# Performance work log

Hardware: AMD Instinct MI355X
Metric: run time of the kernel (lower is better)

## Reference

```python
import jax, jax.numpy as jnp
import numpy as np

N = 20000        # nodes
E = 160000       # directed edges (before self loops)
NODE_DIM = 1287
HEADS = 4
C1, C2, C3 = 128, 256, 128
ACT_SLOPE = 0.15   # module's LeakyReLU between layers
GAT_SLOPE = 0.2    # PyG GATConv default negative_slope


def _gat_layer(x, src, dst, W, att_src, att_dst, bias, heads, out_dim, concat):
    # x: [N, in] ; W: [in, heads*out] ; att_*: [heads, out] ; bias: [heads*out] or [out]
    h = (x @ W).reshape(N, heads, out_dim)                      # [N, H, C]
    a_s = jnp.einsum('nhc,hc->nh', h, att_src)                  # [N, H]
    a_d = jnp.einsum('nhc,hc->nh', h, att_dst)                  # [N, H]
    e = jax.nn.leaky_relu(a_s[src] + a_d[dst], GAT_SLOPE)       # [Etot, H]
    # segment softmax over incoming edges of each dst node (self loops => no empty segments)
    m = jax.ops.segment_max(e, dst, num_segments=N)             # [N, H]
    w = jnp.exp(e - m[dst])
    den = jax.ops.segment_sum(w, dst, num_segments=N)           # [N, H]
    alpha = w / den[dst]                                        # [Etot, H]
    msg = h[src] * alpha[:, :, None]                            # [Etot, H, C]
    out = jax.ops.segment_sum(msg, dst, num_segments=N)         # [N, H, C]
    out = out.reshape(N, heads * out_dim) if concat else out.mean(axis=1)
    return out + bias


def setup_inputs() -> dict:
    key = jax.random.key(0)
    ks = jax.random.split(key, 22)
    s = 0.05
    x = jax.random.normal(ks[0], (N, NODE_DIM), jnp.float32)
    edge_index = jax.random.randint(ks[1], (2, E), 0, N, dtype=jnp.int64)
    inp = {
        'x': x, 'edge_index': edge_index,
        'W1': jax.random.normal(ks[2], (NODE_DIM, HEADS * C1), jnp.float32) * s,
        'as1': jax.random.normal(ks[3], (HEADS, C1), jnp.float32) * s,
        'ad1': jax.random.normal(ks[4], (HEADS, C1), jnp.float32) * s,
        'b1': jnp.zeros((HEADS * C1,), jnp.float32),
        'W2': jax.random.normal(ks[5], (HEADS * C1, HEADS * C2), jnp.float32) * s,
        'as2': jax.random.normal(ks[6], (HEADS, C2), jnp.float32) * s,
        'ad2': jax.random.normal(ks[7], (HEADS, C2), jnp.float32) * s,
        'b2': jnp.zeros((HEADS * C2,), jnp.float32),
        # conv3: 1024 -> 128, 1 head, no concat
        'W3': jax.random.normal(ks[8], (HEADS * C2, C3), jnp.float32) * s,
        'as3': jax.random.normal(ks[9], (1, C3), jnp.float32) * s,
        'ad3': jax.random.normal(ks[10], (1, C3), jnp.float32) * s,
        'b3': jnp.zeros((C3,), jnp.float32),
        # pre_fc: 128 -> 16
        'pw': jax.random.normal(ks[11], (C3, 16), jnp.float32) * s,
        'pb': jnp.zeros((16,), jnp.float32),
        # fc fallback: Linear(16,32) -> LeakyReLU(0.15) -> Linear(32,2)
        'f1w': jax.random.normal(ks[12], (16, 32), jnp.float32) * s,
        'f1b': jnp.zeros((32,), jnp.float32),
        'f2w': jax.random.normal(ks[13], (32, 2), jnp.float32) * s,
        'f2b': jnp.zeros((2,), jnp.float32),
    }
    return inp


def reference(x, edge_index, W1, as1, ad1, b1, W2, as2, ad2, b2,
              W3, as3, ad3, b3, pw, pb, f1w, f1b, f2w, f2b):
    loop = jnp.arange(N, dtype=edge_index.dtype)
    src = jnp.concatenate([edge_index[0], loop])   # PyG add_self_loops=True
    dst = jnp.concatenate([edge_index[1], loop])
    h = _gat_layer(x, src, dst, W1, as1, ad1, b1, HEADS, C1, True)
    h = jax.nn.leaky_relu(h, ACT_SLOPE)            # dropout = identity (eval)
    h = _gat_layer(h, src, dst, W2, as2, ad2, b2, HEADS, C2, True)
    h = jax.nn.leaky_relu(h, ACT_SLOPE)
    h = _gat_layer(h, src, dst, W3, as3, ad3, b3, 1, C3, False)
    h = jax.nn.leaky_relu(h, ACT_SLOPE)
    h = h @ pw + pb                                 # pre_fc (128 -> 16)
    h = jax.nn.leaky_relu(h @ f1w + f1b, ACT_SLOPE)
    return h @ f2w + f2b                            # [N, 2] logits
```

## Files before the change

### kernel.cpp

```cpp
#include <hip/hip_runtime.h>
#include <hip/hip_bf16.h>
#include <cstdint>
#include <cstddef>

#define LRELU(x, s) ((x) > 0.f ? (x) : (s) * (x))

typedef __attribute__((ext_vector_type(8))) short bf16x8;
typedef __attribute__((ext_vector_type(4))) float f32x4;

__device__ __forceinline__ float bflo(uint v) { return __uint_as_float(v << 16); }
__device__ __forceinline__ float bfhi(uint v) { return __uint_as_float(v & 0xffff0000u); }
__device__ __forceinline__ ushort f2bf(float f) {
  const uint u = __float_as_uint(f);
  return (ushort)((u + 0x7fffu + ((u >> 16) & 1u)) >> 16);
}

__global__ void cast_pad_rows(const float* __restrict__ in, ushort* __restrict__ out,
                              int rows, int K, int Kp) {
  const int P4 = Kp >> 2;
  const long long idx = (long long)blockIdx.x * blockDim.x + threadIdx.x;
  if (idx >= (long long)rows * P4) return;
  const int r = (int)(idx / P4);
  const int c = ((int)(idx - (long long)r * P4)) << 2;
  const float* p = in + (size_t)r * K + c;
  float v0 = 0.f, v1 = 0.f, v2 = 0.f, v3 = 0.f;
  if (c + 3 < K) { v0 = p[0]; v1 = p[1]; v2 = p[2]; v3 = p[3]; }
  else {
    if (c + 0 < K) v0 = p[0];
    if (c + 1 < K) v1 = p[1];
    if (c + 2 < K) v2 = p[2];
    if (c + 3 < K) v3 = p[3];
  }
  uint2 o;
  o.x = (uint)f2bf(v0) | ((uint)f2bf(v1) << 16);
  o.y = (uint)f2bf(v2) | ((uint)f2bf(v3) << 16);
  *(uint2*)(out + (size_t)r * Kp + c) = o;
}

__global__ void cast_W_T(const float* __restrict__ W, ushort* __restrict__ Wt,
                         int K, int Nn, int Kp) {
  __shared__ float tile[32][33];
  const int kt = blockIdx.x * 32;
  const int nt = blockIdx.y * 32;
  const int tx = threadIdx.x;
  const int ty = threadIdx.y;
  for (int r = ty; r < 32; r += 8) {
    const int k = kt + r, nn = nt + tx;
    tile[r][tx] = (k < K && nn < Nn) ? W[(size_t)k * Nn + nn] : 0.f;
  }
  __syncthreads();
  for (int r = ty; r < 32; r += 8) {
    const int nn = nt + r, k = kt + tx;
    if (nn < Nn && k < Kp) Wt[(size_t)nn * Kp + k] = f2bf(tile[tx][r]);
  }
}

__global__ __launch_bounds__(256) void gemm_bf16(
    const ushort* __restrict__ A, const ushort* __restrict__ Bt, ushort* __restrict__ C,
    int M, int N, int Kp) {
  constexpr int LDA = 40;
  __shared__ ushort sA[128 * LDA];
  __shared__ ushort sB[128 * LDA];
  const int tid = threadIdx.x;
  const int wave = tid >> 6;
  const int lane = tid & 63;
  const int tilesN = N >> 7;
  const int bx = blockIdx.x % tilesN;
  const int by = blockIdx.x / tilesN;
  const int srow = tid >> 2;
  const int sseg = (tid & 3) * 8;
  const int wrow = (wave >> 1) * 64;
  const int wcol = (wave & 1) * 64;
  const int quad = lane >> 4;
  const int ml = lane & 15;

  const int rA1 = min(by * 128 + srow, M - 1);
  const int rA2 = min(by * 128 + srow + 64, M - 1);
  const int cB1 = bx * 128 + srow;
  const size_t offA1 = (size_t)rA1 * Kp + sseg;
  const size_t offA2 = (size_t)rA2 * Kp + sseg;
  const size_t offB1 = (size_t)cB1 * Kp + sseg;
  const size_t offB2 = (size_t)(cB1 + 64) * Kp + sseg;

  f32x4 acc[4][4];
#pragma unroll
  for (int mi = 0; mi < 4; mi++)
#pragma unroll
    for (int ni = 0; ni < 4; ni++)
#pragma unroll
      for (int e = 0; e < 4; e++) acc[mi][ni][e] = 0.f;

  for (int k0 = 0; k0 < Kp; k0 += 32) {
    const uint4 a1 = *(const uint4*)(A + offA1 + k0);
    const uint4 a2 = *(const uint4*)(A + offA2 + k0);
    const uint4 b1 = *(const uint4*)(Bt + offB1 + k0);
    const uint4 b2 = *(const uint4*)(Bt + offB2 + k0);
    __syncthreads();
    *(uint4*)&sA[srow * LDA + sseg] = a1;
    *(uint4*)&sA[(srow + 64) * LDA + sseg] = a2;
    *(uint4*)&sB[srow * LDA + sseg] = b1;
    *(uint4*)&sB[(srow + 64) * LDA + sseg] = b2;
    __syncthreads();
    bf16x8 af[4], bfr[4];
#pragma unroll
    for (int mi = 0; mi < 4; mi++)
      af[mi] = *(const bf16x8*)&sA[(wrow + mi * 16 + ml) * LDA + quad * 8];
#pragma unroll
    for (int ni = 0; ni < 4; ni++)
      bfr[ni] = *(const bf16x8*)&sB[(wcol + ni * 16 + ml) * LDA + quad * 8];
#pragma unroll
    for (int mi = 0; mi < 4; mi++)
#pragma unroll
      for (int ni = 0; ni < 4; ni++)
        acc[mi][ni] = __builtin_amdgcn_mfma_f32_16x16x32_bf16(af[mi], bfr[ni], acc[mi][ni], 0, 0, 0);
  }

#pragma unroll
  for (int mi = 0; mi < 4; mi++) {
#pragma unroll
    for (int r = 0; r < 4; r++) {
      const int row = by * 128 + wrow + mi * 16 + quad * 4 + r;
      if (row < M) {
#pragma unroll
        for (int ni = 0; ni < 4; ni++) {
          const int col = bx * 128 + wcol + ni * 16 + ml;
          C[(size_t)row * N + col] = f2bf(acc[mi][ni][r]);
        }
      }
    }
  }
}

__global__ void count_deg(const int* __restrict__ dst, int E, int* __restrict__ deg) {
  const int t = blockIdx.x * blockDim.x + threadIdx.x;
  if (t < E) atomicAdd(&deg[dst[t]], 1);
}

__global__ __launch_bounds__(1024) void scan_kernel(const int* __restrict__ deg,
                                                    int* __restrict__ rowptr,
                                                    int* __restrict__ cursor, int n) {
  __shared__ int swsum[16];
  __shared__ int carry_s;
  const int t = threadIdx.x;
  const int wv = t >> 6, lane = t & 63;
  if (t == 0) carry_s = 0;
  __syncthreads();
  for (int base = 0; base < n; base += 1024) {
    const int i = base + t;
    const int v = (i < n) ? (deg[i] + 1) : 0;
    int sc = v;
#pragma unroll
    for (int off = 1; off < 64; off <<= 1) {
      const int u = __shfl_up(sc, off);
      if (lane >= off) sc += u;
    }
    if (lane == 63) swsum[wv] = sc;
    __syncthreads();
    if (t < 16) {
      int x = swsum[t];
#pragma unroll
      for (int off = 1; off < 16; off <<= 1) {
        const int u = __shfl_up(x, off);
        if (t >= off) x += u;
      }
      swsum[t] = x;
    }
    __syncthreads();
    const int incl = sc + (wv == 0 ? 0 : swsum[wv - 1]) + carry_s;
    if (i < n) { rowptr[i + 1] = incl; cursor[i] = incl - v; }
    if (base == 0 && t == 0) rowptr[0] = 0;
    __syncthreads();
    if (t == 0) carry_s += swsum[15];
    __syncthreads();
  }
}

__global__ void scatter_edges(const int* __restrict__ esrc, const int* __restrict__ edst,
                              int E, int Etot, int* __restrict__ cursor,
                              int* __restrict__ csr_src) {
  const int t = blockIdx.x * blockDim.x + threadIdx.x;
  if (t >= Etot) return;
  int s, d;
  if (t < E) { s = esrc[t]; d = edst[t]; } else { s = t - E; d = s; }
  const int pos = atomicAdd(&cursor[d], 1);
  csr_src[pos] = s;
}

template <int H, int C>
__global__ void att_dots_b(const ushort* __restrict__ hb, const float* __restrict__ att_s,
                           const float* __restrict__ att_d, float* __restrict__ a_s,
                           float* __restrict__ a_d, int NH) {
  const int w = blockIdx.x * (blockDim.x >> 6) + (threadIdx.x >> 6);
  const int lane = threadIdx.x & 63;
  if (w >= NH) return;
  const int n = w / H;
  const int h = w - n * H;
  const uint* hp = (const uint*)(hb + (size_t)n * (H * C) + h * C);
  const float2* asp = (const float2*)(att_s + h * C);
  const float2* adp = (const float2*)(att_d + h * C);
  float ss = 0.f, sd = 0.f;
#pragma unroll
  for (int p = lane; p < C / 2; p += 64) {
    const uint v = hp[p];
    const float x0 = bflo(v), x1 = bfhi(v);
    const float2 a = asp[p], b = adp[p];
    ss += x0 * a.x + x1 * a.y;
    sd += x0 * b.x + x1 * b.y;
  }
  for (int off = 32; off > 0; off >>= 1) {
    ss += __shfl_down(ss, off);
    sd += __shfl_down(sd, off);
  }
  if (lane == 0) { a_s[w] = ss; a_d[w] = sd; }
}

template <int H, int C, int TPB, int PPT>
__global__ __launch_bounds__(TPB) void gat_aggregate_b(
    const ushort* __restrict__ hb, const int* __restrict__ rowptr,
    const int* __restrict__ csr_src, const float* __restrict__ a_s,
    const float* __restrict__ a_d, const float* __restrict__ bias,
    ushort* __restrict__ outb, float act_slope) {
  constexpr int HC = H * C;
  constexpr int CH = C / 2;
  constexpr int TILE = 32;
  const int n = blockIdx.x;
  const int tid = threadIdx.x;
  __shared__ int ssrc[TILE];
  __shared__ float sw[TILE * H];
  __shared__ float sden[H];
  if (tid < H) sden[tid] = 0.f;
  float ad_n[H];
#pragma unroll
  for (int h = 0; h < H; h++) ad_n[h] = a_d[n * H + h];
  const int start = rowptr[n], end = rowptr[n + 1];
  float2 acc[PPT];
#pragma unroll
  for (int q = 0; q < PPT; q++) acc[q] = make_float2(0.f, 0.f);

  for (int base = start; base < end; base += TILE) {
    const int cnt = min(TILE, end - base);
    __syncthreads();
    if (tid < cnt) {
      const int s = csr_src[base + tid];
      ssrc[tid] = s;
      float asv[H];
      if constexpr (H == 4) {
        const float4 t4 = *(const float4*)(a_s + s * 4);
        asv[0] = t4.x; asv[1] = t4.y; asv[2] = t4.z; asv[3] = t4.w;
      } else {
#pragma unroll
        for (int h = 0; h < H; h++) asv[h] = a_s[s * H + h];
      }
#pragma unroll
      for (int h = 0; h < H; h++) {
        float lg = asv[h] + ad_n[h];
        lg = LRELU(lg, 0.2f);
        const float w = __expf(lg);
        sw[tid * H + h] = w;
        atomicAdd(&sden[h], w);
      }
    }
    __syncthreads();
    for (int j = 0; j < cnt; j++) {
      const uint* hp = (const uint*)(hb + (size_t)ssrc[j] * HC);
      const float* swj = &sw[j * H];
#pragma unroll
      for (int q = 0; q < PPT; q++) {
        const int p = tid + q * TPB;
        const float w = swj[p / CH];
        const uint v = hp[p];
        acc[q].x += w * bflo(v);
        acc[q].y += w * bfhi(v);
      }
    }
  }
  __syncthreads();
  if (tid < H) sden[tid] = 1.f / sden[tid];
  __syncthreads();
#pragma unroll
  for (int q = 0; q < PPT; q++) {
    const int p = tid + q * TPB;
    const float iv = sden[p / CH];
    const float2 b2 = *(const float2*)(bias + 2 * p);
    const float v0 = LRELU(acc[q].x * iv + b2.x, act_slope);
    const float v1 = LRELU(acc[q].y * iv + b2.y, act_slope);
    ((uint*)outb)[(size_t)n * (HC / 2) + p] = (uint)f2bf(v0) | ((uint)f2bf(v1) << 16);
  }
}

__global__ __launch_bounds__(64) void gat_agg3_mlp(
    const ushort* __restrict__ hb, const int* __restrict__ rowptr,
    const int* __restrict__ csr_src, const float* __restrict__ a_s,
    const float* __restrict__ a_d, const float* __restrict__ b3,
    const float* __restrict__ pw, const float* __restrict__ pb,
    const float* __restrict__ f1w, const float* __restrict__ f1b,
    const float* __restrict__ f2w, const float* __restrict__ f2b,
    float* __restrict__ out) {
  constexpr int TILE = 32;
  const int n = blockIdx.x;
  const int tid = threadIdx.x;
  __shared__ int ssrc[TILE];
  __shared__ float sw[TILE];
  __shared__ float sden1;
  __shared__ float sx[128];
  __shared__ float s1[16];
  __shared__ float s2[32];
  if (tid == 0) sden1 = 0.f;
  const float ad_n = a_d[n];
  const int start = rowptr[n], end = rowptr[n + 1];
  float2 acc = make_float2(0.f, 0.f);
  for (int base = start; base < end; base += TILE) {
    const int cnt = min(TILE, end - base);
    __syncthreads();
    if (tid < cnt) {
      const int s = csr_src[base + tid];
      ssrc[tid] = s;
      float lg = a_s[s] + ad_n;
      lg = LRELU(lg, 0.2f);
      const float w = __expf(lg);
      sw[tid] = w;
      atomicAdd(&sden1, w);
    }
    __syncthreads();
    for (int j = 0; j < cnt; j++) {
      const uint v = ((const uint*)(hb + (size_t)ssrc[j] * 128))[tid];
      const float w = sw[j];
      acc.x += w * bflo(v);
      acc.y += w * bfhi(v);
    }
  }
  __syncthreads();
  const float iv = 1.f / sden1;
  sx[2 * tid]     = LRELU(acc.x * iv + b3[2 * tid], 0.15f);
  sx[2 * tid + 1] = LRELU(acc.y * iv + b3[2 * tid + 1], 0.15f);
  __syncthreads();
  if (tid < 16) {
    float a = pb[tid];
    for (int c = 0; c < 128; c++) a += sx[c] * pw[c * 16 + tid];
    s1[tid] = a;
  }
  __syncthreads();
  if (tid < 32) {
    float a = f1b[tid];
    for (int c = 0; c < 16; c++) a += s1[c] * f1w[c * 32 + tid];
    s2[tid] = LRELU(a, 0.15f);
  }
  __syncthreads();
  if (tid < 2) {
    float a = f2b[tid];
    for (int c = 0; c < 32; c++) a += s2[c] * f2w[c * 2 + tid];
    out[(size_t)n * 2 + tid] = a;
  }
}

extern "C" void kernel_launch(void* const* d_in, const int* in_sizes, int n_in,
                              void* d_out, int out_size, void* d_ws, size_t ws_size,
                              hipStream_t stream) {
  const float* x   = (const float*)d_in[0];
  const int* ei    = (const int*)d_in[1];
  const float* W1  = (const float*)d_in[2];
  const float* as1 = (const float*)d_in[3];
  const float* ad1 = (const float*)d_in[4];
  const float* b1  = (const float*)d_in[5];
  const float* W2  = (const float*)d_in[6];
  const float* as2 = (const float*)d_in[7];
  const float* ad2 = (const float*)d_in[8];
  const float* b2  = (const float*)d_in[9];
  const float* W3  = (const float*)d_in[10];
  const float* as3 = (const float*)d_in[11];
  const float* ad3 = (const float*)d_in[12];
  const float* b3  = (const float*)d_in[13];
  const float* pw  = (const float*)d_in[14];
  const float* pb  = (const float*)d_in[15];
  const float* f1w = (const float*)d_in[16];
  const float* f1b = (const float*)d_in[17];
  const float* f2w = (const float*)d_in[18];
  const float* f2b = (const float*)d_in[19];
  float* out = (float*)d_out;

  const int N = in_sizes[0] / 1287;
  const int E = in_sizes[1] / 2;
  const int Etot = E + N;
  const int* esrc = ei;
  const int* edst = ei + E;
  const int K1 = 1287, K1p = 1312;

  char* ws = (char*)d_ws;
  size_t off = 0;
  auto alloc = [&](size_t bytes) -> void* {
    void* p = ws + off;
    off = (off + bytes + 255) & ~(size_t)255;
    return p;
  };
  ushort* hb  = (ushort*)alloc((size_t)N * 1024 * 2);
  ushort* ob  = (ushort*)alloc((size_t)N * 1024 * 2);
  ushort* xb  = (ushort*)alloc((size_t)N * K1p * 2);
  ushort* W1t = (ushort*)alloc((size_t)512 * K1p * 2);
  ushort* W2t = (ushort*)alloc((size_t)1024 * 512 * 2);
  ushort* W3t = (ushort*)alloc((size_t)128 * 1024 * 2);
  float* as_buf = (float*)alloc((size_t)N * 4 * sizeof(float));
  float* ad_buf = (float*)alloc((size_t)N * 4 * sizeof(float));
  int* deg    = (int*)alloc((size_t)N * sizeof(int));
  int* rowptr = (int*)alloc((size_t)(N + 1) * sizeof(int));
  int* cursor = (int*)alloc((size_t)N * sizeof(int));
  int* csr    = (int*)alloc((size_t)Etot * sizeof(int));

  hipMemsetAsync(deg, 0, (size_t)N * sizeof(int), stream);
  count_deg<<<(E + 255) / 256, 256, 0, stream>>>(edst, E, deg);
  scan_kernel<<<1, 1024, 0, stream>>>(deg, rowptr, cursor, N);
  scatter_edges<<<(Etot + 255) / 256, 256, 0, stream>>>(esrc, edst, E, Etot, cursor, csr);

  {
    const long long nx = (long long)N * (K1p / 4);
    cast_pad_rows<<<(int)((nx + 255) / 256), 256, 0, stream>>>(x, xb, N, K1, K1p);
    cast_W_T<<<dim3(K1p / 32, (512 + 31) / 32), dim3(32, 8), 0, stream>>>(W1, W1t, K1, 512, K1p);
    cast_W_T<<<dim3(512 / 32, 1024 / 32), dim3(32, 8), 0, stream>>>(W2, W2t, 512, 1024, 512);
    cast_W_T<<<dim3(1024 / 32, 128 / 32), dim3(32, 8), 0, stream>>>(W3, W3t, 1024, 128, 1024);
  }

  const int tilesM = (N + 127) / 128;

  {
    const int H = 4, C = 128, HC = 512;
    gemm_bf16<<<tilesM * (HC / 128), 256, 0, stream>>>(xb, W1t, hb, N, HC, K1p);
    const int NH = N * H;
    att_dots_b<4, 128><<<(NH + 3) / 4, 256, 0, stream>>>(hb, as1, ad1, as_buf, ad_buf, NH);
    gat_aggregate_b<4, 128, 256, 1><<<N, 256, 0, stream>>>(hb, rowptr, csr, as_buf, ad_buf,
                                                           b1, ob, 0.15f);
  }
  {
    const int H = 4, C = 256, HC = 1024;
    gemm_bf16<<<tilesM * (HC / 128), 256, 0, stream>>>(ob, W2t, hb, N, HC, 512);
    const int NH = N * H;
    att_dots_b<4, 256><<<(NH + 3) / 4, 256, 0, stream>>>(hb, as2, ad2, as_buf, ad_buf, NH);
    gat_aggregate_b<4, 256, 256, 2><<<N, 256, 0, stream>>>(hb, rowptr, csr, as_buf, ad_buf,
                                                           b2, ob, 0.15f);
  }
  {
    const int HC = 128;
    gemm_bf16<<<tilesM * (HC / 128), 256, 0, stream>>>(ob, W3t, hb, N, HC, 1024);
    att_dots_b<1, 128><<<(N + 3) / 4, 256, 0, stream>>>(hb, as3, ad3, as_buf, ad_buf, N);
    gat_agg3_mlp<<<N, 64, 0, stream>>>(hb, rowptr, csr, as_buf, ad_buf, b3,
                                       pw, pb, f1w, f1b, f2w, f2b, out);
  }
}
```

Baseline: 540.3 us.

## Fuse attention dot products into GEMM epilogue and use wave-per-node aggregation

Attention logit dot products are now computed in the GEMM epilogue from fp32 accumulators, reduced with lane shuffles and atomically added into zeroed buffers. This removes the separate att_dots kernels and their reread of h. Aggregation now runs one wave per node with register-held edge weights broadcast by shuffles, replacing shared memory, block barriers and shared atomics. The cost is extra memsets and global atomics, plus slightly different rounding because the dots use fp32 accumulators rather than bf16 h.

Measured after the change: 542.6 us. No clear change (+0.4%).

```diff
diff --git a/kernel.cpp b/kernel.cpp
--- a/kernel.cpp
+++ b/kernel.cpp
@@ -57,7 +57,9 @@
 
 __global__ __launch_bounds__(256) void gemm_bf16(
     const ushort* __restrict__ A, const ushort* __restrict__ Bt, ushort* __restrict__ C,
-    int M, int N, int Kp) {
+    int M, int N, int Kp,
+    const float* __restrict__ AS, const float* __restrict__ AD,
+    float* __restrict__ asb, float* __restrict__ adb, int H, int headC) {
   constexpr int LDA = 40;
   __shared__ ushort sA[128 * LDA];
   __shared__ ushort sB[128 * LDA];
@@ -129,6 +131,39 @@
       }
     }
   }
+
+  if (asb != nullptr) {
+    float asv[4], adv[4];
+#pragma unroll
+    for (int ni = 0; ni < 4; ni++) {
+      const int col = bx * 128 + wcol + ni * 16 + ml;
+      asv[ni] = AS[col];
+      adv[ni] = AD[col];
+    }
+    const int hh = (bx * 128 + wcol) / headC;
+#pragma unroll
+    for (int mi = 0; mi < 4; mi++) {
+#pragma unroll
+      for (int r = 0; r < 4; r++) {
+        float ps = acc[mi][0][r] * asv[0] + acc[mi][1][r] * asv[1] +
+                   acc[mi][2][r] * asv[2] + acc[mi][3][r] * asv[3];
+        float pd = acc[mi][0][r] * adv[0] + acc[mi][1][r] * adv[1] +
+                   acc[mi][2][r] * adv[2] + acc[mi][3][r] * adv[3];
+#pragma unroll
+        for (int off = 1; off < 16; off <<= 1) {
+          ps += __shfl_xor(ps, off);
+          pd += __shfl_xor(pd, off);
+        }
+        if (ml == 0) {
+          const int row = by * 128 + wrow + mi * 16 + quad * 4 + r;
+          if (row < M) {
+            atomicAdd(&asb[row * H + hh], ps);
+            atomicAdd(&adb[row * H + hh], pd);
+          }
+        }
+      }
+    }
+  }
 }
 
 __global__ void count_deg(const int* __restrict__ dst, int E, int* __restrict__ deg) {
@@ -187,104 +222,90 @@
 }
 
 template <int H, int C>
-__global__ void att_dots_b(const ushort* __restrict__ hb, const float* __restrict__ att_s,
-                           const float* __restrict__ att_d, float* __restrict__ a_s,
-                           float* __restrict__ a_d, int NH) {
-  const int w = blockIdx.x * (blockDim.x >> 6) + (threadIdx.x >> 6);
-  const int lane = threadIdx.x & 63;
-  if (w >= NH) return;
-  const int n = w / H;
-  const int h = w - n * H;
-  const uint* hp = (const uint*)(hb + (size_t)n * (H * C) + h * C);
-  const float2* asp = (const float2*)(att_s + h * C);
-  const float2* adp = (const float2*)(att_d + h * C);
-  float ss = 0.f, sd = 0.f;
-#pragma unroll
-  for (int p = lane; p < C / 2; p += 64) {
-    const uint v = hp[p];
-    const float x0 = bflo(v), x1 = bfhi(v);
-    const float2 a = asp[p], b = adp[p];
-    ss += x0 * a.x + x1 * a.y;
-    sd += x0 * b.x + x1 * b.y;
-  }
-  for (int off = 32; off > 0; off >>= 1) {
-    ss += __shfl_down(ss, off);
-    sd += __shfl_down(sd, off);
-  }
-  if (lane == 0) { a_s[w] = ss; a_d[w] = sd; }
-}
-
-template <int H, int C, int TPB, int PPT>
-__global__ __launch_bounds__(TPB) void gat_aggregate_b(
+__global__ __launch_bounds__(256) void gat_agg_wave(
     const ushort* __restrict__ hb, const int* __restrict__ rowptr,
     const int* __restrict__ csr_src, const float* __restrict__ a_s,
     const float* __restrict__ a_d, const float* __restrict__ bias,
-    ushort* __restrict__ outb, float act_slope) {
+    ushort* __restrict__ outb, float act_slope, int Nn) {
   constexpr int HC = H * C;
-  constexpr int CH = C / 2;
-  constexpr int TILE = 32;
-  const int n = blockIdx.x;
-  const int tid = threadIdx.x;
-  __shared__ int ssrc[TILE];
-  __shared__ float sw[TILE * H];
-  __shared__ float sden[H];
-  if (tid < H) sden[tid] = 0.f;
+  constexpr int NU = HC / 2;
+  constexpr int PPT = NU / 128;
+  const int n = blockIdx.x * 4 + (threadIdx.x >> 6);
+  const int lane = threadIdx.x & 63;
+  if (n >= Nn) return;
   float ad_n[H];
 #pragma unroll
   for (int h = 0; h < H; h++) ad_n[h] = a_d[n * H + h];
   const int start = rowptr[n], end = rowptr[n + 1];
-  float2 acc[PPT];
-#pragma unroll
-  for (int q = 0; q < PPT; q++) acc[q] = make_float2(0.f, 0.f);
-
-  for (int base = start; base < end; base += TILE) {
-    const int cnt = min(TILE, end - base);
-    __syncthreads();
-    if (tid < cnt) {
-      const int s = csr_src[base + tid];
-      ssrc[tid] = s;
+  f32x4 acc[PPT];
+#pragma unroll
+  for (int q = 0; q < PPT; q++)
+#pragma unroll
+    for (int e = 0; e < 4; e++) acc[q][e] = 0.f;
+  float den[H];
+#pragma unroll
+  for (int h = 0; h < H; h++) den[h] = 0.f;
+
+  for (int base = start; base < end; base += 64) {
+    const int cnt = min(64, end - base);
+    int s = 0;
+    float w[H];
+#pragma unroll
+    for (int h = 0; h < H; h++) w[h] = 0.f;
+    if (lane < cnt) {
+      s = csr_src[base + lane];
       float asv[H];
       if constexpr (H == 4) {
         const float4 t4 = *(const float4*)(a_s + s * 4);
         asv[0] = t4.x; asv[1] = t4.y; asv[2] = t4.z; asv[3] = t4.w;
       } else {
-#pragma unroll
-        for (int h = 0; h < H; h++) asv[h] = a_s[s * H + h];
+        asv[0] = a_s[s];
       }
 #pragma unroll
       for (int h = 0; h < H; h++) {
         float lg = asv[h] + ad_n[h];
         lg = LRELU(lg, 0.2f);
-        const float w = __expf(lg);
-        sw[tid * H + h] = w;
-        atomicAdd(&sden[h], w);
-      }
-    }
-    __syncthreads();
+        w[h] = __expf(lg);
+        den[h] += w[h];
+      }
+    }
     for (int j = 0; j < cnt; j++) {
-      const uint* hp = (const uint*)(hb + (size_t)ssrc[j] * HC);
-      const float* swj = &sw[j * H];
+      const int sj = __shfl(s, j);
+      float wj[H];
+#pragma unroll
+      for (int h = 0; h < H; h++) wj[h] = __shfl(w[h], j);
+      const uint2* hp = (const uint2*)(hb + (size_t)sj * HC);
 #pragma unroll
       for (int q = 0; q < PPT; q++) {
-        const int p = tid + q * TPB;
-        const float w = swj[p / CH];
-        const uint v = hp[p];
-        acc[q].x += w * bflo(v);
-        acc[q].y += w * bfhi(v);
-      }
-    }
-  }
-  __syncthreads();
-  if (tid < H) sden[tid] = 1.f / sden[tid];
-  __syncthreads();
+        const int pu = q * 128 + lane * 2;
+        const uint2 v = hp[q * 64 + lane];
+        const float wq = wj[(2 * pu) / C];
+        acc[q][0] += wq * bflo(v.x);
+        acc[q][1] += wq * bfhi(v.x);
+        acc[q][2] += wq * bflo(v.y);
+        acc[q][3] += wq * bfhi(v.y);
+      }
+    }
+  }
+#pragma unroll
+  for (int h = 0; h < H; h++) {
+#pragma unroll
+    for (int off = 1; off < 64; off <<= 1) den[h] += __shfl_xor(den[h], off);
+    den[h] = 1.f / den[h];
+  }
 #pragma unroll
   for (int q = 0; q < PPT; q++) {
-    const int p = tid + q * TPB;
-    const float iv = sden[p / CH];
-    const float2 b2 = *(const float2*)(bias + 2 * p);
-    const float v0 = LRELU(acc[q].x * iv + b2.x, act_slope);
-    const float v1 = LRELU(acc[q].y * iv + b2.y, act_slope);
-    ((uint*)outb)[(size_t)n * (HC / 2) + p] = (uint)f2bf(v0) | ((uint)f2bf(v1) << 16);
+    const int pu = q * 128 + lane * 2;
+    const float iv = den[(2 * pu) / C];
+    const float4 b4 = *(const float4*)(bias + 2 * pu);
+    const float o0 = LRELU(acc[q][0] * iv + b4.x, act_slope);
+    const float o1 = LRELU(acc[q][1] * iv + b4.y, act_slope);
+    const float o2 = LRELU(acc[q][2] * iv + b4.z, act_slope);
+    const float o3 = LRELU(acc[q][3] * iv + b4.w, act_slope);
+    uint2 o;
+    o.x = (uint)f2bf(o0) | ((uint)f2bf(o1) << 16);
+    o.y = (uint)f2bf(o2) | ((uint)f2bf(o3) << 16);
+    ((uint2*)outb)[(size_t)n * (NU / 2) + q * 64 + lane] = o;
   }
 }
 
@@ -296,41 +317,37 @@
     const float* __restrict__ f1w, const float* __restrict__ f1b,
     const float* __restrict__ f2w, const float* __restrict__ f2b,
     float* __restrict__ out) {
-  constexpr int TILE = 32;
   const int n = blockIdx.x;
   const int tid = threadIdx.x;
-  __shared__ int ssrc[TILE];
-  __shared__ float sw[TILE];
-  __shared__ float sden1;
   __shared__ float sx[128];
   __shared__ float s1[16];
   __shared__ float s2[32];
-  if (tid == 0) sden1 = 0.f;
   const float ad_n = a_d[n];
   const int start = rowptr[n], end = rowptr[n + 1];
   float2 acc = make_float2(0.f, 0.f);
-  for (int base = start; base < end; base += TILE) {
-    const int cnt = min(TILE, end - base);
-    __syncthreads();
+  float den = 0.f;
+  for (int base = start; base < end; base += 64) {
+    const int cnt = min(64, end - base);
+    int s = 0;
+    float w = 0.f;
     if (tid < cnt) {
-      const int s = csr_src[base + tid];
-      ssrc[tid] = s;
+      s = csr_src[base + tid];
       float lg = a_s[s] + ad_n;
       lg = LRELU(lg, 0.2f);
-      const float w = __expf(lg);
-      sw[tid] = w;
-      atomicAdd(&sden1, w);
-    }
-    __syncthreads();
+      w = __expf(lg);
+      den += w;
+    }
     for (int j = 0; j < cnt; j++) {
-      const uint v = ((const uint*)(hb + (size_t)ssrc[j] * 128))[tid];
-      const float w = sw[j];
-      acc.x += w * bflo(v);
-      acc.y += w * bfhi(v);
-    }
-  }
-  __syncthreads();
-  const float iv = 1.f / sden1;
+      const int sj = __shfl(s, j);
+      const float wj = __shfl(w, j);
+      const uint v = ((const uint*)(hb + (size_t)sj * 128))[tid];
+      acc.x += wj * bflo(v);
+      acc.y += wj * bfhi(v);
+    }
+  }
+#pragma unroll
+  for (int off = 1; off < 64; off <<= 1) den += __shfl_xor(den, off);
+  const float iv = 1.f / den;
   sx[2 * tid]     = LRELU(acc.x * iv + b3[2 * tid], 0.15f);
   sx[2 * tid + 1] = LRELU(acc.y * iv + b3[2 * tid + 1], 0.15f);
   __syncthreads();
@@ -398,12 +415,13 @@
   ushort* W1t = (ushort*)alloc((size_t)512 * K1p * 2);
   ushort* W2t = (ushort*)alloc((size_t)1024 * 512 * 2);
   ushort* W3t = (ushort*)alloc((size_t)128 * 1024 * 2);
-  float* as_buf = (float*)alloc((size_t)N * 4 * sizeof(float));
-  float* ad_buf = (float*)alloc((size_t)N * 4 * sizeof(float));
+  float* av   = (float*)alloc((size_t)N * 8 * sizeof(float));
   int* deg    = (int*)alloc((size_t)N * sizeof(int));
   int* rowptr = (int*)alloc((size_t)(N + 1) * sizeof(int));
   int* cursor = (int*)alloc((size_t)N * sizeof(int));
   int* csr    = (int*)alloc((size_t)Etot * sizeof(int));
+  float* asb = av;
+  float* adb = av + (size_t)N * 4;
 
   hipMemsetAsync(deg, 0, (size_t)N * sizeof(int), stream);
   count_deg<<<(E + 255) / 256, 256, 0, stream>>>(edst, E, deg);
@@ -419,28 +437,30 @@
   }
 
   const int tilesM = (N + 127) / 128;
+  const int aggBlocks = (N + 3) / 4;
 
   {
     const int H = 4, C = 128, HC = 512;
-    gemm_bf16<<<tilesM * (HC / 128), 256, 0, stream>>>(xb, W1t, hb, N, HC, K1p);
-    const int NH = N * H;
-    att_dots_b<4, 128><<<(NH + 3) / 4, 256, 0, stream>>>(hb, as1, ad1, as_buf, ad_buf, NH);
-    gat_aggregate_b<4, 128, 256, 1><<<N, 256, 0, stream>>>(hb, rowptr, csr, as_buf, ad_buf,
-                                                           b1, ob, 0.15f);
+    hipMemsetAsync(av, 0, (size_t)N * 8 * sizeof(float), stream);
+    gemm_bf16<<<tilesM * (HC / 128), 256, 0, stream>>>(xb, W1t, hb, N, HC, K1p,
+                                                       as1, ad1, asb, adb, H, C);
+    gat_agg_wave<4, 128><<<aggBlocks, 256, 0, stream>>>(hb, rowptr, csr, asb, adb,
+                                                        b1, ob, 0.15f, N);
   }
   {
     const int H = 4, C = 256, HC = 1024;
-    gemm_bf16<<<tilesM * (HC / 128), 256, 0, stream>>>(ob, W2t, hb, N, HC, 512);
-    const int NH = N * H;
-    att_dots_b<4, 256><<<(NH + 3) / 4, 256, 0, stream>>>(hb, as2, ad2, as_buf, ad_buf, NH);
-    gat_aggregate_b<4, 256, 256, 2><<<N, 256, 0, stream>>>(hb, rowptr, csr, as_buf, ad_buf,
-                                                           b2, ob, 0.15f);
+    hipMemsetAsync(av, 0, (size_t)N * 8 * sizeof(float), stream);
+    gemm_bf16<<<tilesM * (HC / 128), 256, 0, stream>>>(ob, W2t, hb, N, HC, 512,
+                                                       as2, ad2, asb, adb, H, C);
+    gat_agg_wave<4, 256><<<aggBlocks, 256, 0, stream>>>(hb, rowptr, csr, asb, adb,
+                                                        b2, ob, 0.15f, N);
   }
   {
     const int HC = 128;
-    gemm_bf16<<<tilesM * (HC / 128), 256, 0, stream>>>(ob, W3t, hb, N, HC, 1024);
-    att_dots_b<1, 128><<<(N + 3) / 4, 256, 0, stream>>>(hb, as3, ad3, as_buf, ad_buf, N);
-    gat_agg3_mlp<<<N, 64, 0, stream>>>(hb, rowptr, csr, as_buf, ad_buf, b3,
+    hipMemsetAsync(av, 0, (size_t)N * 8 * sizeof(float), stream);
+    gemm_bf16<<<tilesM * (HC / 128), 256, 0, stream>>>(ob, W3t, hb, N, HC, 1024,
+                                                       as3, ad3, asb, adb, 1, 128);
+    gat_agg3_mlp<<<N, 64, 0, stream>>>(hb, rowptr, csr, asb, adb, b3,
                                        pw, pb, f1w, f1b, f2w, f2b, out);
   }
 }
```
